# Optimization experiments

Measured on AMD Instinct MI355X. Metric: run time of the kernel, lower is better.

Reference implementation:

```python
import jax, jax.numpy as jnp
import numpy as np

O_FEAT = 4096
I_FEAT = 4096
NNZ = int(0.05 * O_FEAT * I_FEAT)  # 838860, matches k = int(residual.numel()*ortho_ratio)


def setup_inputs() -> dict:
    key = jax.random.key(0)
    k_x, k_pk, k_sc, k_v, k_r, k_c = jax.random.split(key, 6)
    x = jax.random.normal(k_x, (2, 1024, I_FEAT), dtype=jnp.float32)
    # packed int4 weights: each byte holds two 4-bit codes (offset-by-8 signed int4)
    base_packed = jax.random.randint(k_pk, (O_FEAT, I_FEAT // 2), 0, 256).astype(jnp.uint8)
    # per-output-row scales (robust_max / 7), strictly positive
    scales = jax.random.uniform(k_sc, (O_FEAT,), minval=1e-4, maxval=2e-2, dtype=jnp.float32)
    # sparse residual correction in fp16 (CSR values; represented as COO triplets)
    ortho_vals = (jax.random.normal(k_v, (NNZ,), dtype=jnp.float32) * 1e-2).astype(jnp.float16)
    ortho_rows = jax.random.randint(k_r, (NNZ,), 0, O_FEAT, dtype=jnp.int32)
    ortho_cols = jax.random.randint(k_c, (NNZ,), 0, I_FEAT, dtype=jnp.int32)
    return {
        "x": x,
        "base_packed": base_packed,
        "scales": scales,
        "ortho_vals": ortho_vals,
        "ortho_rows": ortho_rows,
        "ortho_cols": ortho_cols,
        "alpha": 1.0,
    }


def _dequant_int4(base_packed, scales):
    # unpack: low nibble -> even columns, high nibble -> odd columns
    O, Ih = base_packed.shape
    low = (base_packed & jnp.uint8(0x0F)).astype(jnp.int32)
    high = (base_packed >> 4).astype(jnp.int32)
    q = jnp.stack([low, high], axis=-1).reshape(O, Ih * 2)  # interleaved [l0,h0,l1,h1,...]
    return (q - 8).astype(jnp.float32) * scales[:, None]


def reference(x, base_packed, scales, ortho_vals, ortho_rows, ortho_cols, alpha):
    O, I = base_packed.shape[0], base_packed.shape[1] * 2
    w_base = _dequant_int4(base_packed, scales)  # [O, I] f32
    # scatter sparse residual into dense weight (same math as CSR spmm residual)
    w_sparse = jnp.zeros((O, I), jnp.float32).at[ortho_rows, ortho_cols].add(
        ortho_vals.astype(jnp.float32))
    W = w_base + alpha * w_sparse
    out = jnp.einsum("bsi,oi->bso", x.astype(jnp.float32), W)
    return out.astype(x.dtype)
```

## Files before the change

### kernel.cpp

```cpp
#include <hip/hip_runtime.h>
#include <hip/hip_fp16.h>
#include <stdint.h>

#define O_FEAT 4096
#define I_FEAT 4096
#define M_DIM  2048
#define K_DIM  4096

typedef __attribute__((ext_vector_type(8))) short short8;
typedef __attribute__((ext_vector_type(2))) short short2v;
typedef __attribute__((ext_vector_type(4))) float floatx4;

#define AS1 __attribute__((address_space(1)))
#define AS3 __attribute__((address_space(3)))

__device__ __forceinline__ uint16_t f32_to_bf16(float f) {
    uint32_t u = __builtin_bit_cast(uint32_t, f);
    u = (u + 0x7FFFu + ((u >> 16) & 1u)) >> 16;
    return (uint16_t)u;
}
__device__ __forceinline__ float bf16_to_f32(uint16_t h) {
    uint32_t u = ((uint32_t)h) << 16;
    return __builtin_bit_cast(float, u);
}

__device__ __forceinline__ void load_lds16(const uint16_t* gptr, uint16_t* ldsptr) {
    __builtin_amdgcn_global_load_lds((const AS1 uint32_t*)gptr,
                                     (AS3 uint32_t*)ldsptr, 16, 0, 0);
}

__global__ __launch_bounds__(256) void dequant_kernel(
        const void*  __restrict__ packed,
        const float* __restrict__ scales,
        uint16_t*    __restrict__ W) {
    const int lane = threadIdx.x & 63;
    uint32_t probe = ((const uint32_t*)packed)[lane];
    const bool int32mode = (__ballot(probe >= 256u) == 0ull);

    int idx = blockIdx.x * 256 + threadIdx.x;
    float s = scales[idx >> 9];

    uint32_t bytes4;
    if (int32mode) {
        uint4 w = ((const uint4*)packed)[idx];
        bytes4 = (w.x & 0xFFu) | ((w.y & 0xFFu) << 8) |
                 ((w.z & 0xFFu) << 16) | ((w.w & 0xFFu) << 24);
    } else {
        bytes4 = ((const uint32_t*)packed)[idx];
    }

    uint16_t o[8];
#pragma unroll
    for (int b = 0; b < 4; ++b) {
        int byte = (bytes4 >> (8 * b)) & 0xFF;
        o[2 * b]     = f32_to_bf16((float)((byte & 0xF) - 8) * s);
        o[2 * b + 1] = f32_to_bf16((float)((byte >> 4) - 8) * s);
    }
    uint4 v;
    v.x = (uint32_t)o[0] | ((uint32_t)o[1] << 16);
    v.y = (uint32_t)o[2] | ((uint32_t)o[3] << 16);
    v.z = (uint32_t)o[4] | ((uint32_t)o[5] << 16);
    v.w = (uint32_t)o[6] | ((uint32_t)o[7] << 16);
    ((uint4*)W)[idx] = v;
}

#define SCATTER_BLOCKS 3328
__global__ __launch_bounds__(256) void scatter_xconv_kernel(
        const void*  __restrict__ vals,
        const int*   __restrict__ rows,
        const int*   __restrict__ cols,
        const float* __restrict__ alpha,
        const float* __restrict__ x,
        uint16_t*    __restrict__ W,
        uint16_t*    __restrict__ Xb,
        int nnz) {
    if (blockIdx.x < SCATTER_BLOCKS) {
        const int lane = threadIdx.x & 63;
        float p = fabsf(((const float*)vals)[lane]);
        int cnt = __popcll(__ballot(p > 1e-4f && p < 1.0f));
        const bool f32mode = (cnt >= 32);

        int i = blockIdx.x * 256 + threadIdx.x;
        if (i >= nnz) return;
        float v = f32mode ? ((const float*)vals)[i]
                          : __half2float(((const __half*)vals)[i]);
        v *= alpha[0];
        int r = rows[i], c = cols[i];
        size_t elem = (size_t)r * I_FEAT + c;

#if __has_builtin(__builtin_amdgcn_global_atomic_fadd_v2bf16)
        const bool hi = (elem & 1);
        short b = (short)f32_to_bf16(v);
        short2v val;
        val[0] = hi ? (short)0 : b;
        val[1] = hi ? b : (short)0;
        __builtin_amdgcn_global_atomic_fadd_v2bf16(
            (AS1 short2v*)(W + (elem & ~(size_t)1)), val);
#else
        uint32_t* word = (uint32_t*)W + (elem >> 1);
        bool hi = (c & 1);
        uint32_t old = *word, assumed;
        do {
            assumed = old;
            uint16_t cur = hi ? (uint16_t)(assumed >> 16) : (uint16_t)(assumed & 0xFFFF);
            uint16_t nw  = f32_to_bf16(bf16_to_f32(cur) + v);
            uint32_t neww = hi ? ((assumed & 0x0000FFFFu) | ((uint32_t)nw << 16))
                               : ((assumed & 0xFFFF0000u) | (uint32_t)nw);
            old = atomicCAS(word, assumed, neww);
        } while (old != assumed);
#endif
    } else {
        int idx = (blockIdx.x - SCATTER_BLOCKS) * 256 + threadIdx.x;
        float4 v0 = ((const float4*)x)[2 * idx];
        float4 v1 = ((const float4*)x)[2 * idx + 1];
        uint4 o;
        o.x = (uint32_t)f32_to_bf16(v0.x) | ((uint32_t)f32_to_bf16(v0.y) << 16);
        o.y = (uint32_t)f32_to_bf16(v0.z) | ((uint32_t)f32_to_bf16(v0.w) << 16);
        o.z = (uint32_t)f32_to_bf16(v1.x) | ((uint32_t)f32_to_bf16(v1.y) << 16);
        o.w = (uint32_t)f32_to_bf16(v1.z) | ((uint32_t)f32_to_bf16(v1.w) << 16);
        ((uint4*)Xb)[idx] = o;
    }
}

__global__ __launch_bounds__(256, 2) void gemm_bt_kernel(
        const uint16_t* __restrict__ A,
        const uint16_t* __restrict__ B,
        float* __restrict__ C) {
    __shared__ uint16_t As[128 * 32];
    __shared__ uint16_t Bs[128 * 32];

    const int tid  = threadIdx.x;
    const int wave = tid >> 6;
    const int lane = tid & 63;
    const int wm = wave >> 1, wn = wave & 1;
    const int bm0 = blockIdx.y * 128;
    const int bn0 = blockIdx.x * 128;

    const int lrow = lane >> 2;
    const int lcol = (lane & 3) * 8;

    floatx4 acc[4][4];
#pragma unroll
    for (int i = 0; i < 4; ++i)
#pragma unroll
        for (int j = 0; j < 4; ++j) acc[i][j] = {0.f, 0.f, 0.f, 0.f};

    const int fr = lane & 15;
    const int ko = (lane >> 4) * 8;

    for (int k0 = 0; k0 < K_DIM; k0 += 32) {
        __syncthreads();
#pragma unroll
        for (int j = 0; j < 2; ++j) {
            const int chunk = wave * 2 + j;
            const int row = chunk * 16 + lrow;
            load_lds16(A + (size_t)(bm0 + row) * K_DIM + k0 + lcol,
                       &As[chunk * 512]);
            load_lds16(B + (size_t)(bn0 + row) * K_DIM + k0 + lcol,
                       &Bs[chunk * 512]);
        }
        __syncthreads();

        short8 af[4], bf[4];
#pragma unroll
        for (int i = 0; i < 4; ++i) {
            af[i] = *(const short8*)&As[(wm * 64 + i * 16 + fr) * 32 + ko];
            bf[i] = *(const short8*)&Bs[(wn * 64 + i * 16 + fr) * 32 + ko];
        }
#pragma unroll
        for (int i = 0; i < 4; ++i)
#pragma unroll
            for (int j = 0; j < 4; ++j)
                acc[i][j] = __builtin_amdgcn_mfma_f32_16x16x32_bf16(
                    af[i], bf[j], acc[i][j], 0, 0, 0);
    }

    const int cn = lane & 15;
    const int rb = (lane >> 4) * 4;
#pragma unroll
    for (int i = 0; i < 4; ++i)
#pragma unroll
        for (int j = 0; j < 4; ++j)
#pragma unroll
            for (int r = 0; r < 4; ++r) {
                const int row = bm0 + wm * 64 + i * 16 + rb + r;
                const int col = bn0 + wn * 64 + j * 16 + cn;
                C[(size_t)row * O_FEAT + col] = acc[i][j][r];
            }
}

extern "C" void kernel_launch(void* const* d_in, const int* in_sizes, int n_in,
                              void* d_out, int out_size, void* d_ws, size_t ws_size,
                              hipStream_t stream) {
    const float* x      = (const float*)d_in[0];
    const void*  packed = d_in[1];
    const float* scales = (const float*)d_in[2];
    const void*  vals   = d_in[3];
    const int*   rows   = (const int*)d_in[4];
    const int*   cols   = (const int*)d_in[5];
    const float* alpha  = (const float*)d_in[6];
    float*       out    = (float*)d_out;
    const int nnz = in_sizes[3];

    uint16_t* W  = (uint16_t*)d_ws;
    uint16_t* Xb = (uint16_t*)((char*)d_ws + (size_t)O_FEAT * I_FEAT * 2);

    dequant_kernel<<<8192, 256, 0, stream>>>(packed, scales, W);
    scatter_xconv_kernel<<<SCATTER_BLOCKS + 4096, 256, 0, stream>>>(
        vals, rows, cols, alpha, x, W, Xb, nnz);
    gemm_bt_kernel<<<dim3(O_FEAT / 128, M_DIM / 128), 256, 0, stream>>>(Xb, W, out);
}
```

Baseline: 246.4 us.

## Rewrite GEMM with 128x256x64 tiles, triple-buffered LDS prefetch and swizzling

Replaces the simple 128x128x32 GEMM, which synchronises twice per k-step, with a 512-thread 128x256 tile kernel over BK=64. Global-to-LDS loads go into a three-stage ring buffer and are issued two tiles ahead, interleaved with four MFMA phases separated by barriers and raised s_setprio. It adds an XOR-swizzled LDS layout to avoid bank conflicts and a workgroup-ID remap for cache locality. The aim is to hide memory latency and raise MFMA utilisation, at the cost of more LDS (144 KB per block) and complex barrier and waitcnt ordering that could break correctness or occupancy.

Result: faster. 230.3 us (-6.5%).

```diff
diff --git a/kernel.cpp b/kernel.cpp
--- a/kernel.cpp
+++ b/kernel.cpp
@@ -122,22 +122,54 @@
     }
 }
 
-__global__ __launch_bounds__(256, 2) void gemm_bt_kernel(
+#define BM 128
+#define BN 256
+#define BK 64
+#define NT (K_DIM / BK)
+#define A_ELEMS (BM * BK)
+#define B_ELEMS (BN * BK)
+#define TILE_ELEMS (A_ELEMS + B_ELEMS)
+
+#define MFMA16(d, a, b) d = __builtin_amdgcn_mfma_f32_16x16x32_bf16(a, b, d, 0, 0, 0)
+
+__global__ __launch_bounds__(512, 2) void gemm_bt_kernel(
         const uint16_t* __restrict__ A,
         const uint16_t* __restrict__ B,
         float* __restrict__ C) {
-    __shared__ uint16_t As[128 * 32];
-    __shared__ uint16_t Bs[128 * 32];
+    __shared__ uint16_t lds[3 * TILE_ELEMS];
 
     const int tid  = threadIdx.x;
     const int wave = tid >> 6;
     const int lane = tid & 63;
-    const int wm = wave >> 1, wn = wave & 1;
-    const int bm0 = blockIdx.y * 128;
-    const int bn0 = blockIdx.x * 128;
-
-    const int lrow = lane >> 2;
-    const int lcol = (lane & 3) * 8;
+    const int wm   = wave >> 2;
+    const int wn   = wave & 3;
+
+    const int wgid = blockIdx.y * 16 + blockIdx.x;
+    const int swz  = (wgid & 7) * 32 + (wgid >> 3);
+    const int bm0  = (swz >> 4) * BM;
+    const int bn0  = (swz & 15) * BN;
+
+    const int srow = (wave << 3) + (lane >> 3);
+    const int xcol = ((lane & 7) ^ (lane >> 3)) << 3;
+    const uint16_t* gA0 = A + (size_t)(bm0 + srow) * K_DIM + xcol;
+    const uint16_t* gA1 = gA0 + (size_t)64 * K_DIM;
+    const uint16_t* gB0 = B + (size_t)(bn0 + srow) * K_DIM + xcol;
+    const uint16_t* gB1 = gB0 + (size_t)64  * K_DIM;
+    const uint16_t* gB2 = gB0 + (size_t)128 * K_DIM;
+    const uint16_t* gB3 = gB0 + (size_t)192 * K_DIM;
+    const int ldsA0 = wave * 512;
+    const int ldsA1 = 4096 + wave * 512;
+    const int ldsB0 = A_ELEMS + wave * 512;
+    const int ldsB1 = A_ELEMS + 4096 + wave * 512;
+    const int ldsB2 = A_ELEMS + 8192 + wave * 512;
+    const int ldsB3 = A_ELEMS + 12288 + wave * 512;
+
+    const int fr  = lane & 15;
+    const int ko  = (lane >> 4) << 3;
+    const int sk0 = (ko)      ^ ((fr & 7) << 3);
+    const int sk1 = (32 + ko) ^ ((fr & 7) << 3);
+    const int raA = (wm * 64 + fr) * BK;
+    const int raB = A_ELEMS + (wn * 64 + fr) * BK;
 
     floatx4 acc[4][4];
 #pragma unroll
@@ -145,45 +177,112 @@
 #pragma unroll
         for (int j = 0; j < 4; ++j) acc[i][j] = {0.f, 0.f, 0.f, 0.f};
 
-    const int fr = lane & 15;
-    const int ko = (lane >> 4) * 8;
-
-    for (int k0 = 0; k0 < K_DIM; k0 += 32) {
-        __syncthreads();
-#pragma unroll
-        for (int j = 0; j < 2; ++j) {
-            const int chunk = wave * 2 + j;
-            const int row = chunk * 16 + lrow;
-            load_lds16(A + (size_t)(bm0 + row) * K_DIM + k0 + lcol,
-                       &As[chunk * 512]);
-            load_lds16(B + (size_t)(bn0 + row) * K_DIM + k0 + lcol,
-                       &Bs[chunk * 512]);
+    load_lds16(gA0, &lds[ldsA0]);
+    load_lds16(gA1, &lds[ldsA1]);
+    load_lds16(gB0, &lds[ldsB0]);
+    load_lds16(gB1, &lds[ldsB1]);
+    load_lds16(gB2, &lds[ldsB2]);
+    load_lds16(gB3, &lds[ldsB3]);
+    load_lds16(gA0 + BK, &lds[TILE_ELEMS + ldsA0]);
+    load_lds16(gA1 + BK, &lds[TILE_ELEMS + ldsA1]);
+    load_lds16(gB0 + BK, &lds[TILE_ELEMS + ldsB0]);
+    load_lds16(gB1 + BK, &lds[TILE_ELEMS + ldsB1]);
+    load_lds16(gB2 + BK, &lds[TILE_ELEMS + ldsB2]);
+    load_lds16(gB3 + BK, &lds[TILE_ELEMS + ldsB3]);
+    asm volatile("s_waitcnt vmcnt(6)" ::: "memory");
+    __builtin_amdgcn_s_barrier();
+
+    int cbo = 0;
+    int sbo = 2 * TILE_ELEMS;
+
+    for (int t = 0; t < NT; ++t) {
+        const bool pf   = (t + 2 < NT);
+        const int  kofs = (t + 2) * BK;
+
+        short8 a00 = *(const short8*)&lds[cbo + raA + sk0];
+        short8 a01 = *(const short8*)&lds[cbo + raA + sk1];
+        short8 a10 = *(const short8*)&lds[cbo + raA + 1024 + sk0];
+        short8 a11 = *(const short8*)&lds[cbo + raA + 1024 + sk1];
+        short8 b00 = *(const short8*)&lds[cbo + raB + sk0];
+        short8 b01 = *(const short8*)&lds[cbo + raB + sk1];
+        short8 b10 = *(const short8*)&lds[cbo + raB + 1024 + sk0];
+        short8 b11 = *(const short8*)&lds[cbo + raB + 1024 + sk1];
+        if (pf) {
+            load_lds16(gA0 + kofs, &lds[sbo + ldsA0]);
+            load_lds16(gA1 + kofs, &lds[sbo + ldsA1]);
         }
-        __syncthreads();
-
-        short8 af[4], bf[4];
-#pragma unroll
-        for (int i = 0; i < 4; ++i) {
-            af[i] = *(const short8*)&As[(wm * 64 + i * 16 + fr) * 32 + ko];
-            bf[i] = *(const short8*)&Bs[(wn * 64 + i * 16 + fr) * 32 + ko];
+        __builtin_amdgcn_s_barrier();
+        asm volatile("s_waitcnt lgkmcnt(0)");
+        __builtin_amdgcn_s_setprio(1);
+        MFMA16(acc[0][0], a00, b00); MFMA16(acc[0][0], a01, b01);
+        MFMA16(acc[0][1], a00, b10); MFMA16(acc[0][1], a01, b11);
+        MFMA16(acc[1][0], a10, b00); MFMA16(acc[1][0], a11, b01);
+        MFMA16(acc[1][1], a10, b10); MFMA16(acc[1][1], a11, b11);
+        __builtin_amdgcn_s_setprio(0);
+        __builtin_amdgcn_s_barrier();
+
+        short8 b20 = *(const short8*)&lds[cbo + raB + 2048 + sk0];
+        short8 b21 = *(const short8*)&lds[cbo + raB + 2048 + sk1];
+        short8 b30 = *(const short8*)&lds[cbo + raB + 3072 + sk0];
+        short8 b31 = *(const short8*)&lds[cbo + raB + 3072 + sk1];
+        if (pf) {
+            load_lds16(gB0 + kofs, &lds[sbo + ldsB0]);
+            load_lds16(gB1 + kofs, &lds[sbo + ldsB1]);
         }
-#pragma unroll
-        for (int i = 0; i < 4; ++i)
-#pragma unroll
-            for (int j = 0; j < 4; ++j)
-                acc[i][j] = __builtin_amdgcn_mfma_f32_16x16x32_bf16(
-                    af[i], bf[j], acc[i][j], 0, 0, 0);
+        __builtin_amdgcn_s_barrier();
+        asm volatile("s_waitcnt lgkmcnt(0)");
+        __builtin_amdgcn_s_setprio(1);
+        MFMA16(acc[0][2], a00, b20); MFMA16(acc[0][2], a01, b21);
+        MFMA16(acc[0][3], a00, b30); MFMA16(acc[0][3], a01, b31);
+        MFMA16(acc[1][2], a10, b20); MFMA16(acc[1][2], a11, b21);
+        MFMA16(acc[1][3], a10, b30); MFMA16(acc[1][3], a11, b31);
+        __builtin_amdgcn_s_setprio(0);
+        __builtin_amdgcn_s_barrier();
+
+        short8 a20 = *(const short8*)&lds[cbo + raA + 2048 + sk0];
+        short8 a21 = *(const short8*)&lds[cbo + raA + 2048 + sk1];
+        short8 a30 = *(const short8*)&lds[cbo + raA + 3072 + sk0];
+        short8 a31 = *(const short8*)&lds[cbo + raA + 3072 + sk1];
+        if (pf) {
+            load_lds16(gB2 + kofs, &lds[sbo + ldsB2]);
+            load_lds16(gB3 + kofs, &lds[sbo + ldsB3]);
+        }
+        __builtin_amdgcn_s_barrier();
+        asm volatile("s_waitcnt lgkmcnt(0)");
+        __builtin_amdgcn_s_setprio(1);
+        MFMA16(acc[2][2], a20, b20); MFMA16(acc[2][2], a21, b21);
+        MFMA16(acc[2][3], a20, b30); MFMA16(acc[2][3], a21, b31);
+        MFMA16(acc[3][2], a30, b20); MFMA16(acc[3][2], a31, b21);
+        MFMA16(acc[3][3], a30, b30); MFMA16(acc[3][3], a31, b31);
+        __builtin_amdgcn_s_setprio(0);
+        __builtin_amdgcn_s_barrier();
+
+        __builtin_amdgcn_s_setprio(1);
+        MFMA16(acc[2][0], a20, b00); MFMA16(acc[2][0], a21, b01);
+        MFMA16(acc[2][1], a20, b10); MFMA16(acc[2][1], a21, b11);
+        MFMA16(acc[3][0], a30, b00); MFMA16(acc[3][0], a31, b01);
+        MFMA16(acc[3][1], a30, b10); MFMA16(acc[3][1], a31, b11);
+        __builtin_amdgcn_s_setprio(0);
+        if (t + 2 < NT) {
+            asm volatile("s_waitcnt vmcnt(6)" ::: "memory");
+        } else if (t + 1 < NT) {
+            asm volatile("s_waitcnt vmcnt(0)" ::: "memory");
+        }
+        if (t + 1 < NT) __builtin_amdgcn_s_barrier();
+
+        cbo += TILE_ELEMS; if (cbo == 3 * TILE_ELEMS) cbo = 0;
+        sbo += TILE_ELEMS; if (sbo == 3 * TILE_ELEMS) sbo = 0;
     }
 
-    const int cn = lane & 15;
-    const int rb = (lane >> 4) * 4;
+    const int cn  = lane & 15;
+    const int rb4 = (lane >> 4) * 4;
 #pragma unroll
     for (int i = 0; i < 4; ++i)
 #pragma unroll
         for (int j = 0; j < 4; ++j)
 #pragma unroll
             for (int r = 0; r < 4; ++r) {
-                const int row = bm0 + wm * 64 + i * 16 + rb + r;
+                const int row = bm0 + wm * 64 + i * 16 + rb4 + r;
                 const int col = bn0 + wn * 64 + j * 16 + cn;
                 C[(size_t)row * O_FEAT + col] = acc[i][j][r];
             }
@@ -208,5 +307,5 @@
     dequant_kernel<<<8192, 256, 0, stream>>>(packed, scales, W);
     scatter_xconv_kernel<<<SCATTER_BLOCKS + 4096, 256, 0, stream>>>(
         vals, rows, cols, alpha, x, W, Xb, nnz);
-    gemm_bt_kernel<<<dim3(O_FEAT / 128, M_DIM / 128), 256, 0, stream>>>(Xb, W, out);
-}
+    gemm_bt_kernel<<<dim3(O_FEAT / BN, M_DIM / BM), 512, 0, stream>>>(Xb, W, out);
+}
```

## Rewrite GEMM with 128x256 tiles, triple-buffered LDS and register-prefetched B

Applied to the files above, without the earlier changes.

The bf16 GEMM now uses 512-thread blocks with 128x256 output tiles and BK=64. A is streamed into a triple-buffered, XOR-swizzled LDS ring two steps ahead. B fragments are loaded straight from global memory into double-buffered registers. It also adds a workgroup-id swizzle for L2 locality, s_setprio around the MFMA bursts, and explicit vmcnt waits with a single barrier per k-step. The aim is to hide global-load latency behind MFMA and cut the per-iteration sync overhead, at the cost of more registers and fragile manual waitcnt accounting.

Measured after the change: 305.0 us. 23.8% more time.

```diff
diff --git a/kernel.cpp b/kernel.cpp
--- a/kernel.cpp
+++ b/kernel.cpp
@@ -122,22 +122,100 @@
     }
 }
 
-__global__ __launch_bounds__(256, 2) void gemm_bt_kernel(
+#define BM 128
+#define BN 256
+#define BK 64
+#define NT (K_DIM / BK)
+#define TILE_A (BM * BK)
+
+#define MFMA16(d, a, b) d = __builtin_amdgcn_mfma_f32_16x16x32_bf16(a, b, d, 0, 0, 0)
+
+#define GTILE(BF, tt, cbo_, sbo_)                                             \
+    {                                                                         \
+        short8 a00 = *(const short8*)&lds[(cbo_) + raA + sk0];                \
+        short8 a01 = *(const short8*)&lds[(cbo_) + raA + sk1];                \
+        short8 a10 = *(const short8*)&lds[(cbo_) + raA + 1024 + sk0];         \
+        short8 a11 = *(const short8*)&lds[(cbo_) + raA + 1024 + sk1];         \
+        short8 a20 = *(const short8*)&lds[(cbo_) + raA + 2048 + sk0];         \
+        short8 a21 = *(const short8*)&lds[(cbo_) + raA + 2048 + sk1];         \
+        short8 a30 = *(const short8*)&lds[(cbo_) + raA + 3072 + sk0];         \
+        short8 a31 = *(const short8*)&lds[(cbo_) + raA + 3072 + sk1];         \
+        if ((tt) + 2 < NT) {                                                  \
+            const int kof = ((tt) + 2) * BK;                                  \
+            load_lds16(gA0 + kof, &lds[(sbo_) + ldsA0]);                      \
+            load_lds16(gA1 + kof, &lds[(sbo_) + ldsA1]);                      \
+        }                                                                     \
+        asm volatile("s_waitcnt lgkmcnt(0)");                                 \
+        __builtin_amdgcn_s_setprio(1);                                        \
+        MFMA16(acc[0][0], a00, BF[0][0]); MFMA16(acc[0][0], a01, BF[0][1]);   \
+        MFMA16(acc[0][1], a00, BF[1][0]); MFMA16(acc[0][1], a01, BF[1][1]);   \
+        MFMA16(acc[0][2], a00, BF[2][0]); MFMA16(acc[0][2], a01, BF[2][1]);   \
+        MFMA16(acc[0][3], a00, BF[3][0]); MFMA16(acc[0][3], a01, BF[3][1]);   \
+        MFMA16(acc[1][0], a10, BF[0][0]); MFMA16(acc[1][0], a11, BF[0][1]);   \
+        MFMA16(acc[1][1], a10, BF[1][0]); MFMA16(acc[1][1], a11, BF[1][1]);   \
+        MFMA16(acc[1][2], a10, BF[2][0]); MFMA16(acc[1][2], a11, BF[2][1]);   \
+        MFMA16(acc[1][3], a10, BF[3][0]); MFMA16(acc[1][3], a11, BF[3][1]);   \
+        MFMA16(acc[2][0], a20, BF[0][0]); MFMA16(acc[2][0], a21, BF[0][1]);   \
+        MFMA16(acc[2][1], a20, BF[1][0]); MFMA16(acc[2][1], a21, BF[1][1]);   \
+        MFMA16(acc[2][2], a20, BF[2][0]); MFMA16(acc[2][2], a21, BF[2][1]);   \
+        MFMA16(acc[2][3], a20, BF[3][0]); MFMA16(acc[2][3], a21, BF[3][1]);   \
+        MFMA16(acc[3][0], a30, BF[0][0]); MFMA16(acc[3][0], a31, BF[0][1]);   \
+        MFMA16(acc[3][1], a30, BF[1][0]); MFMA16(acc[3][1], a31, BF[1][1]);   \
+        MFMA16(acc[3][2], a30, BF[2][0]); MFMA16(acc[3][2], a31, BF[2][1]);   \
+        MFMA16(acc[3][3], a30, BF[3][0]); MFMA16(acc[3][3], a31, BF[3][1]);   \
+        __builtin_amdgcn_s_setprio(0);                                        \
+        if ((tt) + 2 < NT) {                                                  \
+            const int kof2 = ((tt) + 2) * BK;                                 \
+            BF[0][0] = *(const short8*)(bp0 + kof2);                          \
+            BF[0][1] = *(const short8*)(bp0 + kof2 + 32);                     \
+            BF[1][0] = *(const short8*)(bp1 + kof2);                          \
+            BF[1][1] = *(const short8*)(bp1 + kof2 + 32);                     \
+            BF[2][0] = *(const short8*)(bp2 + kof2);                          \
+            BF[2][1] = *(const short8*)(bp2 + kof2 + 32);                     \
+            BF[3][0] = *(const short8*)(bp3 + kof2);                          \
+            BF[3][1] = *(const short8*)(bp3 + kof2 + 32);                     \
+             \
+            asm volatile("s_waitcnt vmcnt(10)" ::: "memory");                 \
+        } else if ((tt) + 1 < NT) {                                           \
+            asm volatile("s_waitcnt vmcnt(0)" ::: "memory");                  \
+        }                                                                     \
+        if ((tt) + 1 < NT) __builtin_amdgcn_s_barrier();                      \
+    }
+
+__global__ __launch_bounds__(512, 2) void gemm_bt_kernel(
         const uint16_t* __restrict__ A,
         const uint16_t* __restrict__ B,
         float* __restrict__ C) {
-    __shared__ uint16_t As[128 * 32];
-    __shared__ uint16_t Bs[128 * 32];
+    __shared__ uint16_t lds[3 * TILE_A];
 
     const int tid  = threadIdx.x;
     const int wave = tid >> 6;
     const int lane = tid & 63;
-    const int wm = wave >> 1, wn = wave & 1;
-    const int bm0 = blockIdx.y * 128;
-    const int bn0 = blockIdx.x * 128;
-
-    const int lrow = lane >> 2;
-    const int lcol = (lane & 3) * 8;
+    const int wm   = wave >> 2;
+    const int wn   = wave & 3;
+
+    const int wgid = blockIdx.y * 16 + blockIdx.x;
+    const int swz  = (wgid & 7) * 32 + (wgid >> 3);
+    const int bm0  = (swz >> 4) * BM;
+    const int bn0  = (swz & 15) * BN;
+
+    const int srow = (wave << 3) + (lane >> 3);
+    const int xcol = ((lane & 7) ^ (lane >> 3)) << 3;
+    const uint16_t* gA0 = A + (size_t)(bm0 + srow) * K_DIM + xcol;
+    const uint16_t* gA1 = gA0 + (size_t)64 * K_DIM;
+    const int ldsA0 = wave * 512;
+    const int ldsA1 = 4096 + wave * 512;
+
+    const int fr  = lane & 15;
+    const int ko  = (lane >> 4) << 3;
+    const int sk0 = (ko)      ^ ((fr & 7) << 3);
+    const int sk1 = (32 + ko) ^ ((fr & 7) << 3);
+    const int raA = (wm * 64 + fr) * BK;
+
+    const uint16_t* bp0 = B + (size_t)(bn0 + wn * 64 +  0 + fr) * K_DIM + ko;
+    const uint16_t* bp1 = B + (size_t)(bn0 + wn * 64 + 16 + fr) * K_DIM + ko;
+    const uint16_t* bp2 = B + (size_t)(bn0 + wn * 64 + 32 + fr) * K_DIM + ko;
+    const uint16_t* bp3 = B + (size_t)(bn0 + wn * 64 + 48 + fr) * K_DIM + ko;
 
     floatx4 acc[4][4];
 #pragma unroll
@@ -145,45 +223,45 @@
 #pragma unroll
         for (int j = 0; j < 4; ++j) acc[i][j] = {0.f, 0.f, 0.f, 0.f};
 
-    const int fr = lane & 15;
-    const int ko = (lane >> 4) * 8;
-
-    for (int k0 = 0; k0 < K_DIM; k0 += 32) {
-        __syncthreads();
-#pragma unroll
-        for (int j = 0; j < 2; ++j) {
-            const int chunk = wave * 2 + j;
-            const int row = chunk * 16 + lrow;
-            load_lds16(A + (size_t)(bm0 + row) * K_DIM + k0 + lcol,
-                       &As[chunk * 512]);
-            load_lds16(B + (size_t)(bn0 + row) * K_DIM + k0 + lcol,
-                       &Bs[chunk * 512]);
-        }
-        __syncthreads();
-
-        short8 af[4], bf[4];
-#pragma unroll
-        for (int i = 0; i < 4; ++i) {
-            af[i] = *(const short8*)&As[(wm * 64 + i * 16 + fr) * 32 + ko];
-            bf[i] = *(const short8*)&Bs[(wn * 64 + i * 16 + fr) * 32 + ko];
-        }
-#pragma unroll
-        for (int i = 0; i < 4; ++i)
-#pragma unroll
-            for (int j = 0; j < 4; ++j)
-                acc[i][j] = __builtin_amdgcn_mfma_f32_16x16x32_bf16(
-                    af[i], bf[j], acc[i][j], 0, 0, 0);
-    }
-
-    const int cn = lane & 15;
-    const int rb = (lane >> 4) * 4;
+    short8 bX[4][2], bY[4][2];
+
+    load_lds16(gA0, &lds[ldsA0]);
+    load_lds16(gA1, &lds[ldsA1]);
+    bX[0][0] = *(const short8*)(bp0);      bX[0][1] = *(const short8*)(bp0 + 32);
+    bX[1][0] = *(const short8*)(bp1);      bX[1][1] = *(const short8*)(bp1 + 32);
+    bX[2][0] = *(const short8*)(bp2);      bX[2][1] = *(const short8*)(bp2 + 32);
+    bX[3][0] = *(const short8*)(bp3);      bX[3][1] = *(const short8*)(bp3 + 32);
+    asm volatile("" ::: "memory");
+    load_lds16(gA0 + BK, &lds[TILE_A + ldsA0]);
+    load_lds16(gA1 + BK, &lds[TILE_A + ldsA1]);
+    bY[0][0] = *(const short8*)(bp0 + BK); bY[0][1] = *(const short8*)(bp0 + BK + 32);
+    bY[1][0] = *(const short8*)(bp1 + BK); bY[1][1] = *(const short8*)(bp1 + BK + 32);
+    bY[2][0] = *(const short8*)(bp2 + BK); bY[2][1] = *(const short8*)(bp2 + BK + 32);
+    bY[3][0] = *(const short8*)(bp3 + BK); bY[3][1] = *(const short8*)(bp3 + BK + 32);
+    asm volatile("s_waitcnt vmcnt(10)" ::: "memory");
+    __builtin_amdgcn_s_barrier();
+
+    int cbo = 0;
+    int sbo = 2 * TILE_A;
+
+    for (int t = 0; t < NT; t += 2) {
+        GTILE(bX, t, cbo, sbo);
+        cbo += TILE_A; if (cbo == 3 * TILE_A) cbo = 0;
+        sbo += TILE_A; if (sbo == 3 * TILE_A) sbo = 0;
+        GTILE(bY, t + 1, cbo, sbo);
+        cbo += TILE_A; if (cbo == 3 * TILE_A) cbo = 0;
+        sbo += TILE_A; if (sbo == 3 * TILE_A) sbo = 0;
+    }
+
+    const int cn  = lane & 15;
+    const int rb4 = (lane >> 4) * 4;
 #pragma unroll
     for (int i = 0; i < 4; ++i)
 #pragma unroll
         for (int j = 0; j < 4; ++j)
 #pragma unroll
             for (int r = 0; r < 4; ++r) {
-                const int row = bm0 + wm * 64 + i * 16 + rb + r;
+                const int row = bm0 + wm * 64 + i * 16 + rb4 + r;
                 const int col = bn0 + wn * 64 + j * 16 + cn;
                 C[(size_t)row * O_FEAT + col] = acc[i][j][r];
             }
@@ -208,5 +286,5 @@
     dequant_kernel<<<8192, 256, 0, stream>>>(packed, scales, W);
     scatter_xconv_kernel<<<SCATTER_BLOCKS + 4096, 256, 0, stream>>>(
         vals, rows, cols, alpha, x, W, Xb, nnz);
-    gemm_bt_kernel<<<dim3(O_FEAT / 128, M_DIM / 128), 256, 0, stream>>>(Xb, W, out);
-}
+    gemm_bt_kernel<<<dim3(O_FEAT / BN, M_DIM / BM), 512, 0, stream>>>(Xb, W, out);
+}
```
